# Kernel optimization log

Hardware: AMD Instinct MI355X
Metric: run time of the kernel (lower is better)

## Reference

```python
import jax, jax.numpy as jnp
import numpy as np

N = 50000        # nodes
E = 800000       # edges (avg degree 16)
IN_DIM = 256
H = 8            # heads
D = 32           # out_dim per head
T = 4            # edge_type_num
F = 16           # edge_feature_dim
NEG_SLOPE = 0.2


def setup_inputs() -> dict:
    key = jax.random.key(0)
    ks = jax.random.split(key, 9)
    feat = jax.random.normal(ks[0], (N, IN_DIM), dtype=jnp.float32)
    e_pro = jax.random.normal(ks[1], (E, F), dtype=jnp.float32)
    mask = jax.random.uniform(ks[2], (E, T), dtype=jnp.float32)
    W_n = jax.random.normal(ks[3], (IN_DIM, H * D), dtype=jnp.float32) * (1.0 / np.sqrt(IN_DIM))
    attn_l = jax.random.normal(ks[4], (H, D, T), dtype=jnp.float32) * 0.1
    attn_r = jax.random.normal(ks[5], (H, D, T), dtype=jnp.float32) * 0.1
    attn_m = jax.random.normal(ks[6], (H, F, T), dtype=jnp.float32) * 0.1
    src = jax.random.randint(ks[7], (E,), 0, N, dtype=jnp.int32)
    dst = jax.random.randint(ks[8], (E,), 0, N, dtype=jnp.int32)
    return {"feat": feat, "e_pro": e_pro, "mask": mask, "W_n": W_n,
            "attn_l": attn_l, "attn_r": attn_r, "attn_m": attn_m,
            "src": src, "dst": dst}


def reference(feat, e_pro, mask, W_n, attn_l, attn_r, attn_m, src, dst):
    # node projection: [N, H, D]
    feat_src = (feat @ W_n).reshape(N, H, D)

    # per-node attention logits per edge type: [N, H, T]
    el = jnp.einsum("nhd,hdt->nht", feat_src, attn_l)
    er = jnp.einsum("nhd,hdt->nht", feat_src, attn_r)
    # per-edge logits per edge type: [E, H, T]
    em = jnp.einsum("ef,hft->eht", e_pro, attn_m)

    # bmm with edge-type mask [E, T] -> scalar per head: [E, H]
    left = jnp.einsum("eht,et->eh", el[src], mask)
    right = jnp.einsum("eht,et->eh", er[dst], mask)
    em_e = jnp.einsum("eht,et->eh", em, mask)

    e = (left + right + em_e) / 3.0
    e = jnp.where(e > 0, e, NEG_SLOPE * e)  # leaky_relu

    # edge softmax over incoming edges of each dst node (stable)
    e_max = jax.ops.segment_max(e, dst, num_segments=N)          # [N, H]
    e_exp = jnp.exp(e - e_max[dst])                               # [E, H]
    e_sum = jax.ops.segment_sum(e_exp, dst, num_segments=N)      # [N, H]
    a = e_exp / e_sum[dst]                                       # [E, H]

    # u_mul_e + sum aggregation: [E, H, D] -> [N, H, D]
    msg = feat_src[src] * a[:, :, None]
    rst = jax.ops.segment_sum(msg, dst, num_segments=N)

    # cat=True: concat heads
    return rst.reshape(N, H * D)
```

## Files before the change

### kernel.cpp

```cpp
#include <hip/hip_runtime.h>
#include <hip/hip_bf16.h>
#include <hip/hip_fp16.h>

#define NN 50000
#define NEDGE 800000
#define INDIM 256
#define NH 8
#define ND 32
#define HD 256
#define NT 4
#define NF 16

typedef __attribute__((ext_vector_type(8))) short s16x8;
typedef __attribute__((ext_vector_type(4))) float f32x4;
typedef unsigned short u16;

__device__ __forceinline__ float bf2f(u16 u) {
    return __uint_as_float(((unsigned int)u) << 16);
}
__device__ __forceinline__ u16 f2bf(float f) {
    __hip_bfloat16 h = __float2bfloat16(f);
    return *reinterpret_cast<u16*>(&h);
}
__device__ __forceinline__ u16 f2h(float f) {
    __half h = __float2half(f);
    return *reinterpret_cast<u16*>(&h);
}
__device__ __forceinline__ float h2f(u16 u) {
    __half h = *reinterpret_cast<__half*>(&u);
    return __half2float(h);
}

__global__ __launch_bounds__(256) void prep_kernel(const float* __restrict__ W,
                                                   u16* __restrict__ Wt,
                                                   int* __restrict__ cnt,
                                                   int* __restrict__ cursor)
{
    int idx = blockIdx.x * 256 + threadIdx.x;
    int k = idx >> 8, c = idx & 255;
    Wt[(size_t)c * 256 + k] = f2bf(W[idx]);
    if (idx < NN) { cnt[idx] = 0; cursor[idx] = 0; }
}

__global__ __launch_bounds__(256) void gemm_mfma(
    const float* __restrict__ feat, const u16* __restrict__ Wt,
    u16* __restrict__ fs, int nrows)
{
    const int tid = threadIdx.x;
    __shared__ u16 At[32 * 256];
    const int brow = blockIdx.x * 32;

    #pragma unroll
    for (int it = 0; it < 4; ++it) {
        int fo = it * 2048 + tid * 8;
        int row = fo >> 8, col = fo & 255;
        int grow = brow + row;
        if (grow >= nrows) grow = nrows - 1;
        const float* gp = feat + (size_t)grow * 256 + col;
        float4 x = *reinterpret_cast<const float4*>(gp);
        float4 y = *reinterpret_cast<const float4*>(gp + 4);
        s16x8 v;
        v[0] = (short)f2bf(x.x); v[1] = (short)f2bf(x.y);
        v[2] = (short)f2bf(x.z); v[3] = (short)f2bf(x.w);
        v[4] = (short)f2bf(y.x); v[5] = (short)f2bf(y.y);
        v[6] = (short)f2bf(y.z); v[7] = (short)f2bf(y.w);
        int byte = (col * 2) ^ ((row & 7) << 4);
        *reinterpret_cast<s16x8*>((char*)At + row * 512 + byte) = v;
    }
    __syncthreads();

    const int wave = tid >> 6, lane = tid & 63;
    const int c0 = wave * 64;
    const int rA = lane & 15;
    const int kg = lane >> 4;

    f32x4 acc[2][4] = {};

    for (int k0 = 0; k0 < 256; k0 += 32) {
        const int kk = k0 + kg * 8;
        const int byte = (kk * 2) ^ ((rA & 7) << 4);
        s16x8 a0 = *reinterpret_cast<const s16x8*>((char*)At + rA * 512 + byte);
        s16x8 a1 = *reinterpret_cast<const s16x8*>((char*)At + (16 + rA) * 512 + byte);
        #pragma unroll
        for (int ct = 0; ct < 4; ++ct) {
            s16x8 b = *reinterpret_cast<const s16x8*>(Wt + (size_t)(c0 + ct * 16 + rA) * 256 + kk);
            acc[0][ct] = __builtin_amdgcn_mfma_f32_16x16x32_bf16(a0, b, acc[0][ct], 0, 0, 0);
            acc[1][ct] = __builtin_amdgcn_mfma_f32_16x16x32_bf16(a1, b, acc[1][ct], 0, 0, 0);
        }
    }

    #pragma unroll
    for (int rt = 0; rt < 2; ++rt) {
        #pragma unroll
        for (int r = 0; r < 4; ++r) {
            int row = brow + rt * 16 + kg * 4 + r;
            if (row < nrows) {
                #pragma unroll
                for (int ct = 0; ct < 4; ++ct) {
                    fs[(size_t)row * 256 + c0 + ct * 16 + rA] = f2bf(acc[rt][ct][r]);
                }
            }
        }
    }
}

__global__ __launch_bounds__(256) void elr_kernel(
    const u16* __restrict__ fs,
    const float* __restrict__ attn_l, const float* __restrict__ attn_r,
    u16* __restrict__ el, u16* __restrict__ er,
    const int* __restrict__ dst, int* __restrict__ cnt, int n, int ne)
{
    __shared__ float s_al[NH * ND * NT];
    __shared__ float s_ar[NH * ND * NT];

    int gid = blockIdx.x * 256 + threadIdx.x;
    if (gid < ne) atomicAdd(&cnt[dst[gid]], 1);

    for (int i = threadIdx.x; i < NH * ND * NT; i += 256) {
        s_al[i] = attn_l[i];
        s_ar[i] = attn_r[i];
    }
    __syncthreads();
    int wv = threadIdx.x >> 6, lane = threadIdx.x & 63;
    int node = blockIdx.x * 4 + wv;
    if (node >= n) return;
    int h = lane >> 3, j0 = (lane & 7) * 4;
    ushort4 u = *reinterpret_cast<const ushort4*>(fs + (size_t)node * HD + lane * 4);
    float f0 = bf2f(u.x), f1 = bf2f(u.y), f2 = bf2f(u.z), f3 = bf2f(u.w);
    const float* al = s_al + h * (ND * NT) + j0 * NT;
    const float* ar = s_ar + h * (ND * NT) + j0 * NT;
    float pl[NT], pr[NT];
    #pragma unroll
    for (int t = 0; t < NT; ++t) {
        pl[t] = f0*al[t] + f1*al[NT + t] + f2*al[2*NT + t] + f3*al[3*NT + t];
        pr[t] = f0*ar[t] + f1*ar[NT + t] + f2*ar[2*NT + t] + f3*ar[3*NT + t];
    }
    #pragma unroll
    for (int d = 1; d < 8; d <<= 1) {
        #pragma unroll
        for (int t = 0; t < NT; ++t) {
            pl[t] += __shfl_xor(pl[t], d);
            pr[t] += __shfl_xor(pr[t], d);
        }
    }
    if ((lane & 7) == 0) {
        ushort4 ol, orr;
        ol.x = f2h(pl[0]); ol.y = f2h(pl[1]); ol.z = f2h(pl[2]); ol.w = f2h(pl[3]);
        orr.x = f2h(pr[0]); orr.y = f2h(pr[1]); orr.z = f2h(pr[2]); orr.w = f2h(pr[3]);
        *reinterpret_cast<ushort4*>(el + (size_t)node * (NH*NT) + h * NT) = ol;
        *reinterpret_cast<ushort4*>(er + (size_t)node * (NH*NT) + h * NT) = orr;
    }
}

__global__ void scan1_kernel(const int* __restrict__ cnt, int* __restrict__ off,
                             int* __restrict__ blksum, int n) {
    __shared__ int sm[256];
    int i = blockIdx.x * 256 + threadIdx.x;
    int v = (i < n) ? cnt[i] : 0;
    sm[threadIdx.x] = v;
    __syncthreads();
    for (int d = 1; d < 256; d <<= 1) {
        int t = (threadIdx.x >= d) ? sm[threadIdx.x - d] : 0;
        __syncthreads();
        sm[threadIdx.x] += t;
        __syncthreads();
    }
    if (i < n) off[i] = sm[threadIdx.x] - v;
    if (threadIdx.x == 255) blksum[blockIdx.x] = sm[255];
}

__global__ void scan2_kernel(int* blksum, int nb) {
    __shared__ int sm[256];
    int v = (threadIdx.x < nb) ? blksum[threadIdx.x] : 0;
    sm[threadIdx.x] = v;
    __syncthreads();
    for (int d = 1; d < 256; d <<= 1) {
        int t = (threadIdx.x >= d) ? sm[threadIdx.x - d] : 0;
        __syncthreads();
        sm[threadIdx.x] += t;
        __syncthreads();
    }
    blksum[threadIdx.x] = sm[threadIdx.x] - v;
}

__global__ void scan3_kernel(int* __restrict__ off, const int* __restrict__ blksum,
                             int n, int ne) {
    int i = blockIdx.x * 256 + threadIdx.x;
    if (i < n) off[i] += blksum[blockIdx.x];
    if (i == 0) off[n] = ne;
}

__global__ __launch_bounds__(256) void fill_edge_kernel(
    const float* __restrict__ e_pro, const float* __restrict__ mask,
    const float* __restrict__ attn_m,
    const int* __restrict__ src, const int* __restrict__ dst,
    const u16* __restrict__ el, const u16* __restrict__ er,
    const int* __restrict__ off, int* __restrict__ cursor,
    int2* __restrict__ es, u16* __restrict__ ev, int ne)
{
    const int bid = blockIdx.x;
    const int tid = threadIdx.x;

    if (bid % 9 == 0) {
        int e = (bid / 9) * 256 + tid;
        if (e < ne) {
            int d = dst[e];
            int p = atomicAdd(&cursor[d], 1);
            es[off[d] + p] = make_int2(e, src[e]);
        }
        return;
    }

    const int ebid = bid - 1 - bid / 9;
    __shared__ float4 s_am4[NF][NH];
    __shared__ float s_ep[32][17];
    __shared__ float s_mk[32][5];
    const int eb = ebid * 32;
    const int j = tid & 7;
    const int el_ = (tid >> 3) & 31;
    const int e = eb + (tid >> 3);

    int s = src[e], d = dst[e];
    union { uint2 v; u16 u[4]; } lv, rv;
    lv.v = *reinterpret_cast<const uint2*>(el + (size_t)s * (NH*NT) + j * NT);
    rv.v = *reinterpret_cast<const uint2*>(er + (size_t)d * (NH*NT) + j * NT);

    for (int i = tid; i < NH * NF; i += 256) {
        int h = i >> 4, f = i & 15;
        const float* p = attn_m + (size_t)h * (NF * NT) + f * NT;
        s_am4[f][h] = make_float4(p[0], p[1], p[2], p[3]);
    }
    {
        int f2i = tid * 2;
        float2 v = *reinterpret_cast<const float2*>(e_pro + (size_t)eb * NF + f2i);
        int e_l = f2i >> 4, f = f2i & 15;
        s_ep[e_l][f] = v.x; s_ep[e_l][f + 1] = v.y;
    }
    if (tid < 128) {
        s_mk[tid >> 2][tid & 3] = mask[(size_t)eb * NT + tid];
    }
    __syncthreads();

    float4 mk = make_float4(s_mk[el_][0], s_mk[el_][1], s_mk[el_][2], s_mk[el_][3]);

    float em = 0.f;
    #pragma unroll
    for (int f = 0; f < NF; ++f) {
        float4 am = s_am4[f][j];
        float amm = mk.x*am.x + mk.y*am.y + mk.z*am.z + mk.w*am.w;
        em = fmaf(s_ep[el_][f], amm, em);
    }
    float left  = mk.x*h2f(lv.u[0]) + mk.y*h2f(lv.u[1]) + mk.z*h2f(lv.u[2]) + mk.w*h2f(lv.u[3]);
    float right = mk.x*h2f(rv.u[0]) + mk.y*h2f(rv.u[1]) + mk.z*h2f(rv.u[2]) + mk.w*h2f(rv.u[3]);

    float v = (left + right + em) * (1.0f / 3.0f);
    v = v > 0.f ? v : 0.2f * v;
    ev[(size_t)e * NH + j] = f2h(__expf(v));
}

__global__ __launch_bounds__(256) void agg_kernel(
    const int* __restrict__ off, const int2* __restrict__ es,
    const u16* __restrict__ ev, const u16* __restrict__ fs,
    float* __restrict__ out, int n)
{
    int wv = threadIdx.x >> 6, lane = threadIdx.x & 63;
    int node = blockIdx.x * 4 + wv;
    if (node >= n) return;
    int beg = off[node], end = off[node + 1];
    int deg = end - beg;

    int h = lane & 7, sub = lane >> 3;
    float vc[8];
    int sc[8];
    #pragma unroll
    for (int slot = 0; slot < 8; ++slot) {
        int i = beg + slot * 8 + sub;
        float v = 0.f; int sn = 0;
        if (i < end) {
            int2 p = es[i];
            v = h2f(ev[(size_t)p.x * NH + h]);
            sn = p.y;
        }
        vc[slot] = v; sc[slot] = sn;
    }

    int h2 = lane >> 3;
    const int col = lane * 4;
    float a0 = 0.f, a1 = 0.f, a2 = 0.f, a3 = 0.f, sw = 0.f;
    int deg_ = deg < 64 ? deg : 64;
    int nchunk = (deg_ + 7) >> 3;
    #pragma unroll
    for (int c = 0; c < 8; ++c) {
        if (c >= nchunk) break;
        float w8 = vc[c];
        int s8 = sc[c];
        float w[8]; int sn[8];
        #pragma unroll
        for (int q = 0; q < 8; ++q) {
            w[q]  = __shfl(w8, q * 8 + h2);
            sn[q] = __shfl(s8, q * 8 + h2);
        }
        ushort4 u[8];
        #pragma unroll
        for (int q = 0; q < 8; ++q)
            u[q] = *reinterpret_cast<const ushort4*>(fs + (size_t)sn[q] * HD + col);
        #pragma unroll
        for (int q = 0; q < 8; ++q) {
            sw += w[q];
            a0 = fmaf(w[q], bf2f(u[q].x), a0);
            a1 = fmaf(w[q], bf2f(u[q].y), a1);
            a2 = fmaf(w[q], bf2f(u[q].z), a2);
            a3 = fmaf(w[q], bf2f(u[q].w), a3);
        }
    }
    for (int i = beg + 64; i < end; ++i) {
        int2 p = es[i];
        float w = h2f(ev[(size_t)p.x * NH + h2]);
        sw += w;
        ushort4 u = *reinterpret_cast<const ushort4*>(fs + (size_t)p.y * HD + col);
        a0 = fmaf(w, bf2f(u.x), a0); a1 = fmaf(w, bf2f(u.y), a1);
        a2 = fmaf(w, bf2f(u.z), a2); a3 = fmaf(w, bf2f(u.w), a3);
    }
    float invS = sw > 0.f ? 1.f / sw : 0.f;
    a0 *= invS; a1 *= invS; a2 *= invS; a3 *= invS;
    *reinterpret_cast<float4*>(&out[(size_t)node * HD + col]) = make_float4(a0, a1, a2, a3);
}

extern "C" void kernel_launch(void* const* d_in, const int* in_sizes, int n_in,
                              void* d_out, int out_size, void* d_ws, size_t ws_size,
                              hipStream_t stream)
{
    const float* feat   = (const float*)d_in[0];
    const float* e_pro  = (const float*)d_in[1];
    const float* mask   = (const float*)d_in[2];
    const float* W_n    = (const float*)d_in[3];
    const float* attn_l = (const float*)d_in[4];
    const float* attn_r = (const float*)d_in[5];
    const float* attn_m = (const float*)d_in[6];
    const int* src      = (const int*)d_in[7];
    const int* dst      = (const int*)d_in[8];
    float* out = (float*)d_out;

    char* ws = (char*)d_ws;
    size_t o = 0;
    auto alloc = [&](size_t bytes) -> void* {
        void* p = (void*)(ws + o);
        o += (bytes + 255) & ~(size_t)255;
        return p;
    };
    u16* fs     = (u16*)alloc((size_t)NN * HD * 2);
    u16* Wt     = (u16*)alloc((size_t)INDIM * HD * 2);
    u16* el     = (u16*)alloc((size_t)NN * NH * NT * 2);
    u16* er     = (u16*)alloc((size_t)NN * NH * NT * 2);
    u16* ev     = (u16*)alloc((size_t)NEDGE * NH * 2);
    int2* es    = (int2*)alloc((size_t)NEDGE * 8);
    int* cnt    = (int*)alloc((size_t)NN * 4);
    int* cursor = (int*)alloc((size_t)NN * 4);
    int* offs   = (int*)alloc((size_t)(NN + 1) * 4);
    int* blksum = (int*)alloc(256 * 4);
    (void)ws_size; (void)in_sizes; (void)n_in; (void)out_size;

    dim3 b256(256);
    hipLaunchKernelGGL(prep_kernel, dim3(256), b256, 0, stream, W_n, Wt, cnt, cursor);
    hipLaunchKernelGGL(gemm_mfma, dim3((NN + 31) / 32), b256, 0, stream, feat, Wt, fs, NN);
    hipLaunchKernelGGL(elr_kernel, dim3((NN + 3) / 4), b256, 0, stream,
                       fs, attn_l, attn_r, el, er, dst, cnt, NN, NEDGE);
    hipLaunchKernelGGL(scan1_kernel, dim3((NN + 255) / 256), b256, 0, stream, cnt, offs, blksum, NN);
    hipLaunchKernelGGL(scan2_kernel, dim3(1), b256, 0, stream, blksum, (NN + 255) / 256);
    hipLaunchKernelGGL(scan3_kernel, dim3((NN + 255) / 256), b256, 0, stream, offs, blksum, NN, NEDGE);
    hipLaunchKernelGGL(fill_edge_kernel, dim3(9 * 3125), b256, 0, stream,
                       e_pro, mask, attn_m, src, dst, el, er, offs, cursor, es, ev, NEDGE);
    hipLaunchKernelGGL(agg_kernel, dim3((NN + 3) / 4), b256, 0, stream,
                       offs, es, ev, fs, out, NN);
}
```

Baseline: 237.2 us.

## Split degree histogram into own kernel and load edge features via shuffles

Moves the dst-degree atomic histogram out of elr_kernel into a separate hist_kernel launched before the GEMM, and reorders elr after the scan. In fill_edge, each thread now loads its edge's mask as a float4 and a float2 slice of e_pro directly, sharing e_pro across the 8 head-lanes with wave shuffles instead of staging both through shared memory. This removes two shared arrays and part of the staging work before the barrier, at the cost of one extra kernel launch and redundant mask loads per lane.

New measurement: 242.0 us. 2.1% more time.

```diff
diff --git a/kernel.cpp b/kernel.cpp
--- a/kernel.cpp
+++ b/kernel.cpp
@@ -40,6 +40,11 @@
     int k = idx >> 8, c = idx & 255;
     Wt[(size_t)c * 256 + k] = f2bf(W[idx]);
     if (idx < NN) { cnt[idx] = 0; cursor[idx] = 0; }
+}
+
+__global__ void hist_kernel(const int* __restrict__ dst, int* __restrict__ cnt, int ne) {
+    int e = blockIdx.x * 256 + threadIdx.x;
+    if (e < ne) atomicAdd(&cnt[dst[e]], 1);
 }
 
 __global__ __launch_bounds__(256) void gemm_mfma(
@@ -107,15 +112,10 @@
 __global__ __launch_bounds__(256) void elr_kernel(
     const u16* __restrict__ fs,
     const float* __restrict__ attn_l, const float* __restrict__ attn_r,
-    u16* __restrict__ el, u16* __restrict__ er,
-    const int* __restrict__ dst, int* __restrict__ cnt, int n, int ne)
+    u16* __restrict__ el, u16* __restrict__ er, int n)
 {
     __shared__ float s_al[NH * ND * NT];
     __shared__ float s_ar[NH * ND * NT];
-
-    int gid = blockIdx.x * 256 + threadIdx.x;
-    if (gid < ne) atomicAdd(&cnt[dst[gid]], 1);
-
     for (int i = threadIdx.x; i < NH * ND * NT; i += 256) {
         s_al[i] = attn_l[i];
         s_ar[i] = attn_r[i];
@@ -213,42 +213,32 @@
 
     const int ebid = bid - 1 - bid / 9;
     __shared__ float4 s_am4[NF][NH];
-    __shared__ float s_ep[32][17];
-    __shared__ float s_mk[32][5];
     const int eb = ebid * 32;
     const int j = tid & 7;
-    const int el_ = (tid >> 3) & 31;
     const int e = eb + (tid >> 3);
 
     int s = src[e], d = dst[e];
     union { uint2 v; u16 u[4]; } lv, rv;
     lv.v = *reinterpret_cast<const uint2*>(el + (size_t)s * (NH*NT) + j * NT);
     rv.v = *reinterpret_cast<const uint2*>(er + (size_t)d * (NH*NT) + j * NT);
+    float4 mk = *reinterpret_cast<const float4*>(mask + (size_t)e * NT);
+    float2 myep = *reinterpret_cast<const float2*>(e_pro + (size_t)e * NF + j * 2);
 
     for (int i = tid; i < NH * NF; i += 256) {
         int h = i >> 4, f = i & 15;
-        const float* p = attn_m + (size_t)h * (NF * NT) + f * NT;
-        s_am4[f][h] = make_float4(p[0], p[1], p[2], p[3]);
-    }
-    {
-        int f2i = tid * 2;
-        float2 v = *reinterpret_cast<const float2*>(e_pro + (size_t)eb * NF + f2i);
-        int e_l = f2i >> 4, f = f2i & 15;
-        s_ep[e_l][f] = v.x; s_ep[e_l][f + 1] = v.y;
-    }
-    if (tid < 128) {
-        s_mk[tid >> 2][tid & 3] = mask[(size_t)eb * NT + tid];
-    }
-    __syncthreads();
-
-    float4 mk = make_float4(s_mk[el_][0], s_mk[el_][1], s_mk[el_][2], s_mk[el_][3]);
-
+        s_am4[f][h] = *reinterpret_cast<const float4*>(attn_m + (size_t)h * (NF * NT) + f * NT);
+    }
+    __syncthreads();
+
+    const int gbase = (tid & 63) & 56;
+    float pa = myep.x, pb = myep.y;
     float em = 0.f;
     #pragma unroll
     for (int f = 0; f < NF; ++f) {
         float4 am = s_am4[f][j];
         float amm = mk.x*am.x + mk.y*am.y + mk.z*am.z + mk.w*am.w;
-        em = fmaf(s_ep[el_][f], amm, em);
+        float epv = __shfl((f & 1) ? pb : pa, gbase | (f >> 1));
+        em = fmaf(epv, amm, em);
     }
     float left  = mk.x*h2f(lv.u[0]) + mk.y*h2f(lv.u[1]) + mk.z*h2f(lv.u[2]) + mk.w*h2f(lv.u[3]);
     float right = mk.x*h2f(rv.u[0]) + mk.y*h2f(rv.u[1]) + mk.z*h2f(rv.u[2]) + mk.w*h2f(rv.u[3]);
@@ -362,12 +352,12 @@
 
     dim3 b256(256);
     hipLaunchKernelGGL(prep_kernel, dim3(256), b256, 0, stream, W_n, Wt, cnt, cursor);
+    hipLaunchKernelGGL(hist_kernel, dim3((NEDGE + 255) / 256), b256, 0, stream, dst, cnt, NEDGE);
     hipLaunchKernelGGL(gemm_mfma, dim3((NN + 31) / 32), b256, 0, stream, feat, Wt, fs, NN);
-    hipLaunchKernelGGL(elr_kernel, dim3((NN + 3) / 4), b256, 0, stream,
-                       fs, attn_l, attn_r, el, er, dst, cnt, NN, NEDGE);
     hipLaunchKernelGGL(scan1_kernel, dim3((NN + 255) / 256), b256, 0, stream, cnt, offs, blksum, NN);
     hipLaunchKernelGGL(scan2_kernel, dim3(1), b256, 0, stream, blksum, (NN + 255) / 256);
     hipLaunchKernelGGL(scan3_kernel, dim3((NN + 255) / 256), b256, 0, stream, offs, blksum, NN, NEDGE);
+    hipLaunchKernelGGL(elr_kernel, dim3((NN + 3) / 4), b256, 0, stream, fs, attn_l, attn_r, el, er, NN);
     hipLaunchKernelGGL(fill_edge_kernel, dim3(9 * 3125), b256, 0, stream,
                        e_pro, mask, attn_m, src, dst, el, er, offs, cursor, es, ev, NEDGE);
     hipLaunchKernelGGL(agg_kernel, dim3((NN + 3) / 4), b256, 0, stream,
```
